# Performance work log

Hardware: AMD Instinct MI355X
Metric: run time of the kernel (lower is better)

## Reference

```python
import jax, jax.numpy as jnp
import numpy as np

B, P, D_IN, D_MOD, N_HEADS = 512, 64, 64, 256, 4

def _ln(x, g, b):
    m = x.mean(-1, keepdims=True)
    v = ((x - m) ** 2).mean(-1, keepdims=True)
    return (x - m) / jnp.sqrt(v + 1e-5) * g + b

def _lin(x, w, b):
    return x @ w.T + b

def _mha(q, k, v, in_w, in_b, out_w, out_b, n_heads):
    # Faithful to torch nn.MultiheadAttention(batch_first=False): dim0=seq, dim1=batch.
    S, N, E = q.shape
    dh = E // n_heads
    wq, wk, wv = jnp.split(in_w, 3, axis=0)
    bq, bk, bv = jnp.split(in_b, 3)
    qp = _lin(q, wq, bq).reshape(S, N, n_heads, dh)
    kp = _lin(k, wk, bk).reshape(S, N, n_heads, dh)
    vp = _lin(v, wv, bv).reshape(S, N, n_heads, dh)
    scores = jnp.einsum('snhd,tnhd->nhst', qp, kp) * (1.0 / np.sqrt(dh))
    attn = jax.nn.softmax(scores, axis=-1)
    o = jnp.einsum('nhst,tnhd->snhd', attn, vp).reshape(S, N, E)
    return _lin(o, out_w, out_b)

def _forward(x, emb_w, emb_b, emb_g, emb_beta, post_w, post_b, post_g, post_beta,
             attn_qw, attn_qb, attn_kw, attn_kb, attn_vw, attn_vb,
             attn_inw, attn_inb, attn_outw, attn_outb, attn_g, attn_beta,
             player_w, player_b, player_g, player_beta,
             team_w, team_b, team_g, team_beta,
             pre_w, pre_b, pre_g, pre_beta, lnf_g, lnf_b, pred_w, pred_b):
    # embedding: LinearWithLayerNorm = LayerNorm(Linear(x))
    p = _ln(_lin(x, emb_w, emb_b), emb_g, emb_beta)
    # post_embedding: ResidualLinearWithLayerNorm = LayerNorm(Linear(x)) + x
    p = _ln(_lin(p, post_w, post_b), post_g, post_beta) + p
    for i in range(2):
        res = p
        q = _lin(p, attn_qw[i], attn_qb[i])
        k = _lin(p, attn_kw[i], attn_kb[i])
        v = _lin(p, attn_vw[i], attn_vb[i])
        a = _mha(q, k, v, attn_inw[i], attn_inb[i], attn_outw[i], attn_outb[i], N_HEADS)
        p = _ln(a, attn_g[i], attn_beta[i]) + res
    for i in range(2):
        p = _ln(_lin(p, player_w[i], player_b[i]), player_g[i], player_beta[i]) + p
    # segment reduce: padded-ragged scatter + sum == masked sum over the player axis.
    # NOTE: original code computes BOTH masks as original[:,:,-1]==1 (bug preserved).
    mask = (x[:, :, -1] == 1).astype(p.dtype)  # [B, P]
    home = jnp.einsum('bpd,bp->bd', p, mask)
    away = home
    teams = jnp.concatenate([home, away], axis=1)  # [B, 2*d_mod]
    for i in range(2):
        teams = _ln(_lin(teams, team_w[i], team_b[i]), team_g[i], team_beta[i]) + teams
    o = _ln(_lin(teams, pre_w, pre_b), pre_g, pre_beta)
    o = _ln(o, lnf_g, lnf_b)
    o = _lin(o, pred_w, pred_b)[:, 0]  # squeeze(dim=1)
    return o


def setup_inputs() -> dict:
    key = jax.random.key(0)
    ks = iter(jax.random.split(key, 64))
    def nrm(shape):
        return jax.random.normal(next(ks), shape, jnp.float32) * 0.02
    x = jax.random.normal(next(ks), (B, P, D_IN), jnp.float32)
    flag = jax.random.bernoulli(next(ks), 0.5, (B, P)).astype(jnp.float32)
    x = x.at[:, :, -1].set(flag)  # binary home-team indicator channel
    d, d2 = D_MOD, 2 * D_MOD
    return dict(
        x=x,
        emb_w=nrm((d, D_IN)), emb_b=jnp.zeros(d), emb_g=jnp.ones(d), emb_beta=jnp.zeros(d),
        post_w=nrm((d, d)), post_b=jnp.zeros(d), post_g=jnp.ones(d), post_beta=jnp.zeros(d),
        attn_qw=nrm((2, d, d)), attn_qb=jnp.zeros((2, d)),
        attn_kw=nrm((2, d, d)), attn_kb=jnp.zeros((2, d)),
        attn_vw=nrm((2, d, d)), attn_vb=jnp.zeros((2, d)),
        attn_inw=nrm((2, 3 * d, d)), attn_inb=jnp.zeros((2, 3 * d)),
        attn_outw=nrm((2, d, d)), attn_outb=jnp.zeros((2, d)),
        attn_g=jnp.ones((2, d)), attn_beta=jnp.zeros((2, d)),
        player_w=nrm((2, d, d)), player_b=jnp.zeros((2, d)),
        player_g=jnp.ones((2, d)), player_beta=jnp.zeros((2, d)),
        team_w=nrm((2, d2, d2)), team_b=jnp.zeros((2, d2)),
        team_g=jnp.ones((2, d2)), team_beta=jnp.zeros((2, d2)),
        pre_w=nrm((d, d2)), pre_b=jnp.zeros(d), pre_g=jnp.ones(d), pre_beta=jnp.zeros(d),
        lnf_g=jnp.ones(d), lnf_b=jnp.zeros(d),
        pred_w=nrm((1, d)), pred_b=jnp.zeros(1),
    )


def reference(x, emb_w, emb_b, emb_g, emb_beta, post_w, post_b, post_g, post_beta,
              attn_qw, attn_qb, attn_kw, attn_kb, attn_vw, attn_vb,
              attn_inw, attn_inb, attn_outw, attn_outb, attn_g, attn_beta,
              player_w, player_b, player_g, player_beta,
              team_w, team_b, team_g, team_beta,
              pre_w, pre_b, pre_g, pre_beta, lnf_g, lnf_b, pred_w, pred_b):
    return _forward(x, emb_w, emb_b, emb_g, emb_beta, post_w, post_b, post_g, post_beta,
                    attn_qw, attn_qb, attn_kw, attn_kb, attn_vw, attn_vb,
                    attn_inw, attn_inb, attn_outw, attn_outb, attn_g, attn_beta,
                    player_w, player_b, player_g, player_beta,
                    team_w, team_b, team_g, team_beta,
                    pre_w, pre_b, pre_g, pre_beta, lnf_g, lnf_b, pred_w, pred_b)
```

## Files before the change

### kernel.cpp

```cpp
#include <hip/hip_runtime.h>
#include <math.h>


typedef __bf16 bf16x8 __attribute__((ext_vector_type(8)));
typedef __bf16 bf16x4 __attribute__((ext_vector_type(4)));
typedef __bf16 bf16x2 __attribute__((ext_vector_type(2)));
typedef float  f32x4  __attribute__((ext_vector_type(4)));
typedef unsigned short u16;
typedef unsigned short u16x8 __attribute__((ext_vector_type(8)));

__device__ __forceinline__ u16 f2b(float f) {
    unsigned int u = __builtin_bit_cast(unsigned int, f);
    return (u16)((u + 0x7fffu + ((u >> 16) & 1u)) >> 16);
}
__device__ __forceinline__ float b2f(u16 u) {
    unsigned int v = ((unsigned int)u) << 16;
    return __builtin_bit_cast(float, v);
}
__device__ __forceinline__ bf16x8 ld2x64(const u16* p) {
    bf16x4 lo = *(const bf16x4*)p;
    bf16x4 hi = *(const bf16x4*)(p + 4);
    return __builtin_shufflevector(lo, hi, 0, 1, 2, 3, 4, 5, 6, 7);
}
__device__ __forceinline__ bf16x8 ld4x32(const u16* p) {
    bf16x2 a = *(const bf16x2*)p,     b = *(const bf16x2*)(p + 2);
    bf16x2 c = *(const bf16x2*)(p + 4), d = *(const bf16x2*)(p + 6);
    bf16x4 lo = __builtin_shufflevector(a, b, 0, 1, 2, 3);
    bf16x4 hi = __builtin_shufflevector(c, d, 0, 1, 2, 3);
    return __builtin_shufflevector(lo, hi, 0, 1, 2, 3, 4, 5, 6, 7);
}
__device__ __forceinline__ void split8(const float* __restrict__ s,
                                       bf16x8& hi, bf16x8& lo) {
    u16x8 h, l;
    #pragma unroll
    for (int j = 0; j < 8; ++j) {
        float v  = s[j];
        u16  hb  = f2b(v);
        h[j] = hb;
        l[j] = f2b(v - b2f(hb));
    }
    hi = __builtin_bit_cast(bf16x8, h);
    lo = __builtin_bit_cast(bf16x8, l);
}

template<int IN, bool LN, bool RES, bool AF32, int OMODE, bool TEAM>
__device__ __forceinline__
void gemm_body(const void* __restrict__ Xa, const void* __restrict__ Xb, int ldX,
               const u16* __restrict__ Whi, const u16* __restrict__ Wlo,
               const float* __restrict__ bias,
               const float* __restrict__ g, const float* __restrict__ beta,
               const u16* __restrict__ resh, const u16* __restrict__ resl,
               int ldRes, void* __restrict__ Y0, void* __restrict__ Y1, int ldY,
               const float* __restrict__ xmask, float* __restrict__ teams,
               u16* __restrict__ Wb)
{
    constexpr int KT = IN / 32;
    const int tid = threadIdx.x;
    const int wv = tid >> 6, lane = tid & 63;
    const int quad = lane >> 4, l16 = lane & 15;
    const long arow = (long)blockIdx.x * 64 + wv * 16 + l16;

    const u16* sbase[8];
    int sdst[8];
    #pragma unroll
    for (int i = 0; i < 8; ++i) {
        int cid = tid + i * 256;
        int plane = cid >> 10, nt = (cid >> 6) & 15, slot = cid & 63;
        int q = slot >> 4, c = slot & 15;
        sbase[i] = (plane ? Wlo : Whi) + (long)(nt * 16 + c) * IN + q * 8;
        sdst[i]  = (plane * 16 + nt) * 512 + slot * 8;
    }
    u16x8 wreg[8];
    auto issueW = [&](int kt) {
        #pragma unroll
        for (int i = 0; i < 8; ++i) wreg[i] = *(const u16x8*)(sbase[i] + kt * 32);
    };
    auto commitW = [&](int buf) {
        #pragma unroll
        for (int i = 0; i < 8; ++i)
            *(u16x8*)&Wb[buf * 16384 + sdst[i]] = wreg[i];
    };

    bf16x8 ah[3], al[3];
    auto loadA = [&](int kt) {
        int s = kt % 3;
        long aofs = arow * (long)ldX + kt * 32 + quad * 8;
        if constexpr (AF32) {
            float av[8];
            *(f32x4*)&av[0] = *(const f32x4*)&((const float*)Xa)[aofs];
            *(f32x4*)&av[4] = *(const f32x4*)&((const float*)Xa)[aofs + 4];
            split8(av, ah[s], al[s]);
        } else {
            ah[s] = *(const bf16x8*)&((const u16*)Xa)[aofs];
            al[s] = *(const bf16x8*)&((const u16*)Xb)[aofs];
        }
    };

    f32x4 acc[16];
    #pragma unroll
    for (int nt = 0; nt < 16; ++nt) acc[nt] = f32x4{0.f, 0.f, 0.f, 0.f};

    issueW(0);
    commitW(0);
    if (KT > 1) issueW(1);
    loadA(0);
    if (KT > 1) loadA(1);
    __syncthreads();

    #pragma unroll
    for (int kt = 0; kt < KT; ++kt) {
        if (kt + 2 < KT) loadA(kt + 2);
        const u16* wb = Wb + (kt & 1) * 16384;
        const int s = kt % 3;
        #pragma unroll
        for (int nt = 0; nt < 16; ++nt) {
            bf16x8 bhi = *(const bf16x8*)&wb[nt * 512 + lane * 8];
            bf16x8 blo = *(const bf16x8*)&wb[(16 + nt) * 512 + lane * 8];
            acc[nt] = __builtin_amdgcn_mfma_f32_16x16x32_bf16(al[s], bhi, acc[nt], 0, 0, 0);
            acc[nt] = __builtin_amdgcn_mfma_f32_16x16x32_bf16(ah[s], blo, acc[nt], 0, 0, 0);
            acc[nt] = __builtin_amdgcn_mfma_f32_16x16x32_bf16(ah[s], bhi, acc[nt], 0, 0, 0);
        }
        if (kt + 1 < KT) {
            commitW((kt + 1) & 1);
            if (kt + 2 < KT) issueW(kt + 2);
            __syncthreads();
        }
    }

    #pragma unroll
    for (int nt = 0; nt < 16; ++nt) {
        float bc = bias[nt * 16 + l16];
        #pragma unroll
        for (int r = 0; r < 4; ++r) acc[nt][r] += bc;
    }

    float mean[4], rstd[4];
    if constexpr (LN) {
        float s1[4] = {0, 0, 0, 0}, s2[4] = {0, 0, 0, 0};
        #pragma unroll
        for (int nt = 0; nt < 16; ++nt)
            #pragma unroll
            for (int r = 0; r < 4; ++r) {
                s1[r] += acc[nt][r];
                s2[r] += acc[nt][r] * acc[nt][r];
            }
        #pragma unroll
        for (int off = 1; off < 16; off <<= 1)
            #pragma unroll
            for (int r = 0; r < 4; ++r) {
                s1[r] += __shfl_xor(s1[r], off, 64);
                s2[r] += __shfl_xor(s2[r], off, 64);
            }
        #pragma unroll
        for (int r = 0; r < 4; ++r) {
            mean[r] = s1[r] * (1.0f / 256.f);
            float var = s2[r] * (1.0f / 256.f) - mean[r] * mean[r];
            rstd[r] = rsqrtf(var + 1e-5f);
        }
    }

    if constexpr (TEAM) {
        float m[4];
        #pragma unroll
        for (int r = 0; r < 4; ++r) {
            long row = (long)blockIdx.x * 64 + wv * 16 + quad * 4 + r;
            m[r] = (xmask[row * 64 + 63] == 1.0f) ? 1.0f : 0.0f;
        }
        float ts[16];
        #pragma unroll
        for (int nt = 0; nt < 16; ++nt) {
            int col = nt * 16 + l16;
            float gc = g[col], bc2 = beta[col];
            ts[nt] = 0.f;
            #pragma unroll
            for (int r = 0; r < 4; ++r) {
                long row = (long)blockIdx.x * 64 + wv * 16 + quad * 4 + r;
                float v = (acc[nt][r] - mean[r]) * rstd[r] * gc + bc2;
                v += b2f(resh[row * ldRes + col]) + b2f(resl[row * ldRes + col]);
                ts[nt] += m[r] * v;
            }
        }
        #pragma unroll
        for (int nt = 0; nt < 16; ++nt) {
            ts[nt] += __shfl_xor(ts[nt], 16, 64);
            ts[nt] += __shfl_xor(ts[nt], 32, 64);
        }
        __syncthreads();
        float* tsum = (float*)Wb;
        if (quad == 0) {
            #pragma unroll
            for (int nt = 0; nt < 16; ++nt)
                tsum[wv * 256 + nt * 16 + l16] = ts[nt];
        }
        __syncthreads();
        if (tid < 256) {
            float tot = tsum[tid] + tsum[256 + tid]
                      + tsum[512 + tid] + tsum[768 + tid];
            teams[(long)blockIdx.x * 512 + tid]       = tot;
            teams[(long)blockIdx.x * 512 + 256 + tid] = tot;
        }
        return;
    }

    #pragma unroll
    for (int nt = 0; nt < 16; ++nt) {
        int col = nt * 16 + l16;
        float gc = 1.f, bc2 = 0.f;
        if constexpr (LN) { gc = g[col]; bc2 = beta[col]; }
        #pragma unroll
        for (int r = 0; r < 4; ++r) {
            long row = (long)blockIdx.x * 64 + wv * 16 + quad * 4 + r;
            float v = acc[nt][r];
            if constexpr (LN) v = (v - mean[r]) * rstd[r] * gc + bc2;
            if constexpr (RES)
                v += b2f(resh[row * ldRes + col]) + b2f(resl[row * ldRes + col]);
            long yofs = row * ldY + col;
            if constexpr (OMODE == 0) {
                ((float*)Y0)[yofs] = v;
            } else if constexpr (OMODE == 1) {
                u16 hb = f2b(v);
                ((u16*)Y0)[yofs] = hb;
                ((u16*)Y1)[yofs] = f2b(v - b2f(hb));
            } else if constexpr (OMODE == 2) {
                ((u16*)Y0)[yofs] = f2b(v);
            } else {
                long idx = ((long)((row & 63) * 4 + (col >> 6)) * 512
                            + (row >> 6)) * 64 + (col & 63);
                ((u16*)Y0)[idx] = f2b(v);
            }
        }
    }
}

template<int IN, bool LN, bool RES, bool AF32, int OMODE, bool TEAM>
__global__ __launch_bounds__(256)
void gemm_kernel(const void* __restrict__ Xa, const void* __restrict__ Xb, int ldX,
                 const u16* __restrict__ Whi, const u16* __restrict__ Wlo,
                 const float* __restrict__ bias,
                 const float* __restrict__ g, const float* __restrict__ beta,
                 const u16* __restrict__ resh, const u16* __restrict__ resl,
                 int ldRes, void* __restrict__ Y0, void* __restrict__ Y1, int ldY,
                 const float* __restrict__ xmask, float* __restrict__ teams)
{
    __shared__ u16 Wb[32768];
    gemm_body<IN, LN, RES, AF32, OMODE, TEAM>(Xa, Xb, ldX, Whi, Wlo, bias, g,
                                              beta, resh, resl, ldRes, Y0, Y1,
                                              ldY, xmask, teams, Wb);
}

__global__ __launch_bounds__(256)
void qkv_proj(const u16* __restrict__ ph, const u16* __restrict__ pl,
              const u16* __restrict__ cwL, const float* __restrict__ cb,
              u16* __restrict__ qb, u16* __restrict__ kb, u16* __restrict__ vh)
{
    __shared__ u16 Wb[32768];
    int wsel = blockIdx.y;
    const u16* whi = cwL + (long)wsel * 65536;
    const u16* wlo = cwL + 393216 + (long)wsel * 65536;
    u16* Y = (wsel == 0) ? qb : (wsel == 1) ? kb : vh;
    gemm_body<256, false, false, false, 3, false>(
        ph, pl, 256, whi, wlo, cb + wsel * 256, nullptr, nullptr,
        nullptr, nullptr, 0, Y, nullptr, 256, nullptr, nullptr, Wb);
}

__global__ __launch_bounds__(256)
void combine_kernel(const float* __restrict__ inw, const float* __restrict__ inb,
                    const float* __restrict__ qw, const float* __restrict__ kw,
                    const float* __restrict__ vw, const float* __restrict__ qb,
                    const float* __restrict__ kb, const float* __restrict__ vb,
                    u16* __restrict__ cw, float* __restrict__ cb)
{
    int idx = blockIdx.y, L = idx / 3, wsel = idx % 3;
    const float* Wa = inw + (long)L * 768 * 256 + wsel * 65536;
    const float* ba = inb + L * 768 + wsel * 256;
    const float* Wf = (wsel == 0 ? qw : wsel == 1 ? kw : vw) + (long)L * 65536;
    const float* bf = (wsel == 0 ? qb : wsel == 1 ? kb : vb) + L * 256;

    int o = blockIdx.x, j = threadIdx.x;
    float s = 0.f;
    for (int mm = 0; mm < 256; ++mm)
        s += Wa[o * 256 + mm] * Wf[mm * 256 + j];
    u16 hb = f2b(s);
    cw[(long)idx * 65536 + o * 256 + j] = hb;
    cw[393216 + (long)idx * 65536 + o * 256 + j] = f2b(s - b2f(hb));

    __shared__ float red[256];
    red[j] = Wa[o * 256 + j] * bf[j];
    __syncthreads();
    for (int st = 128; st > 0; st >>= 1) {
        if (j < st) red[j] += red[j + st];
        __syncthreads();
    }
    if (j == 0) cb[idx * 256 + o] = red[0] + ba[o];
}

__global__ __launch_bounds__(256)
void cast_split_multi(const float* s0, u16* d0, int n0,
                      const float* s1, u16* d1, int n1,
                      const float* s2, u16* d2, int n2,
                      const float* s3, u16* d3, int n3,
                      const float* s4, u16* d4, int n4,
                      const float* s5, u16* d5, int n5)
{
    const float* s; u16* d; int n;
    switch (blockIdx.y) {
        case 0: s = s0; d = d0; n = n0; break;
        case 1: s = s1; d = d1; n = n1; break;
        case 2: s = s2; d = d2; n = n2; break;
        case 3: s = s3; d = d3; n = n3; break;
        case 4: s = s4; d = d4; n = n4; break;
        default: s = s5; d = d5; n = n5; break;
    }
    int i = (blockIdx.x * 256 + threadIdx.x) * 4;
    if (i >= n) return;
    float4 v = *(const float4*)&s[i];
// ... 13 lines not shown
__global__ __launch_bounds__(256)
void attn_kernel(const u16* __restrict__ qbuf, const u16* __restrict__ kbuf,
                 const u16* __restrict__ vh,
                 u16* __restrict__ ofh, u16* __restrict__ ofl)
{
    const int n = blockIdx.x, h = blockIdx.y, sq = blockIdx.z;
    const int tid = threadIdx.x;
    const int wv = tid >> 6, lane = tid & 63;
    const int quad = lane >> 4, l16 = lane & 15;
    const long nhb = (long)(n * 4 + h) * 32768;

    __shared__ u16 Vth[64 * VTS];
    __shared__ u16 Pbh[4][32 * PS];

    bf16x8 qf[2][2];
    #pragma unroll
    for (int rt = 0; rt < 2; ++rt)
        #pragma unroll
        for (int kc = 0; kc < 2; ++kc) {
            long s = sq * 128 + wv * 32 + rt * 16 + l16;
            qf[rt][kc] = *(const bf16x8*)&qbuf[nhb + s * 64 + kc * 32 + quad * 8];
        }

    f32x4 o[2][4];
    #pragma unroll
    for (int rt = 0; rt < 2; ++rt)
        #pragma unroll
        for (int dt = 0; dt < 4; ++dt) o[rt][dt] = f32x4{0.f, 0.f, 0.f, 0.f};
    float l_run[2][4] = {{0.f, 0.f, 0.f, 0.f}, {0.f, 0.f, 0.f, 0.f}};

    for (int tb = 0; tb < 8; ++tb) {
        __syncthreads();
        for (int i = tid; i < 512; i += 256) {
            int t = i >> 3, c = i & 7;
            u16x8 hvv = *(const u16x8*)&vh[nhb + (long)(tb * 64 + t) * 64 + c * 8];
            #pragma unroll
            for (int j = 0; j < 8; ++j)
                Vth[(c * 8 + j) * VTS + t] = hvv[j];
        }
        __syncthreads();

        f32x4 sA[2][4];
        #pragma unroll
        for (int rt = 0; rt < 2; ++rt)
            #pragma unroll
            for (int tt = 0; tt < 4; ++tt) sA[rt][tt] = f32x4{0.f, 0.f, 0.f, 0.f};
        #pragma unroll
        for (int kc = 0; kc < 2; ++kc)
            #pragma unroll
            for (int tt = 0; tt < 4; ++tt) {
                bf16x8 kf = *(const bf16x8*)
                    &kbuf[nhb + (long)(tb * 64 + tt * 16 + l16) * 64
                          + kc * 32 + quad * 8];
                sA[0][tt] = __builtin_amdgcn_mfma_f32_16x16x32_bf16(
                    qf[0][kc], kf, sA[0][tt], 0, 0, 0);
                sA[1][tt] = __builtin_amdgcn_mfma_f32_16x16x32_bf16(
                    qf[1][kc], kf, sA[1][tt], 0, 0, 0);
            }

        #pragma unroll
        for (int rt = 0; rt < 2; ++rt)
            #pragma unroll
            for (int r = 0; r < 4; ++r) {
                float p0 = exp2f(sA[rt][0][r] * EXP2SCALE);
                float p1 = exp2f(sA[rt][1][r] * EXP2SCALE);
                float p2 = exp2f(sA[rt][2][r] * EXP2SCALE);
                float p3 = exp2f(sA[rt][3][r] * EXP2SCALE);
                int prow = (rt * 16 + quad * 4 + r) * PS + l16;
                Pbh[wv][prow +  0] = f2b(p0);
                Pbh[wv][prow + 16] = f2b(p1);
                Pbh[wv][prow + 32] = f2b(p2);
                Pbh[wv][prow + 48] = f2b(p3);
                l_run[rt][r] += (p0 + p1) + (p2 + p3);
            }

        #pragma unroll
        for (int kc = 0; kc < 2; ++kc) {
            bf16x8 pfh[2];
            #pragma unroll
            for (int rt = 0; rt < 2; ++rt)
                pfh[rt] = ld2x64(&Pbh[wv][(rt * 16 + l16) * PS
                                          + kc * 32 + quad * 8]);
            #pragma unroll
            for (int dt = 0; dt < 4; ++dt) {
                bf16x8 vfh = ld4x32(&Vth[(dt * 16 + l16) * VTS
                                         + kc * 32 + quad * 8]);
                o[0][dt] = __builtin_amdgcn_mfma_f32_16x16x32_bf16(
                    pfh[0], vfh, o[0][dt], 0, 0, 0);
                o[1][dt] = __builtin_amdgcn_mfma_f32_16x16x32_bf16(
                    pfh[1], vfh, o[1][dt], 0, 0, 0);
            }
        }
    }

    #pragma unroll
    for (int off = 1; off < 16; off <<= 1)
        #pragma unroll
        for (int rt = 0; rt < 2; ++rt)
            #pragma unroll
            for (int r = 0; r < 4; ++r)
                l_run[rt][r] += __shfl_xor(l_run[rt][r], off, 64);

    #pragma unroll
    for (int rt = 0; rt < 2; ++rt)
        #pragma unroll
        for (int r = 0; r < 4; ++r) {
            float inv = 1.0f / l_run[rt][r];
            long s = sq * 128 + wv * 32 + rt * 16 + quad * 4 + r;
            #pragma unroll
            for (int dt = 0; dt < 4; ++dt) {
                long idx = (s * 64 + n) * 256 + h * 64 + dt * 16 + l16;
                float val = o[rt][dt][r] * inv;
                u16 hb = f2b(val);
                ofh[idx] = hb;
                ofl[idx] = f2b(val - b2f(hb));
            }
        }
}

template<int IN, int OUT, bool RES>
__global__ __launch_bounds__(256)
void tail_gemm(const float* __restrict__ X,
               const u16* __restrict__ Whi, const u16* __restrict__ Wlo,
               const float* __restrict__ bias,
               const float* __restrict__ g, const float* __restrict__ beta,
               const float* __restrict__ res, float* __restrict__ Y)
{
    constexpr int NTW = OUT / 64;
    constexpr int KT  = IN / 32;
    const int tid = threadIdx.x;
    const int wv = tid >> 6, lane = tid & 63;
    const int quad = lane >> 4, l16 = lane & 15;
    const int row0 = blockIdx.x * 16;
    const int colbase = wv * (OUT / 4);

    f32x4 acc[NTW];
    #pragma unroll
    for (int nt = 0; nt < NTW; ++nt) acc[nt] = f32x4{0.f, 0.f, 0.f, 0.f};

    #pragma unroll
    for (int kt = 0; kt < KT; ++kt) {
        float av[8];
        long aofs = (long)(row0 + l16) * IN + kt * 32 + quad * 8;
        *(f32x4*)&av[0] = *(const f32x4*)&X[aofs];
        *(f32x4*)&av[4] = *(const f32x4*)&X[aofs + 4];
        bf16x8 ah, al;
        split8(av, ah, al);
        #pragma unroll
        for (int nt = 0; nt < NTW; ++nt) {
            long wofs = (long)(colbase + nt * 16 + l16) * IN + kt * 32 + quad * 8;
            bf16x8 bhi = *(const bf16x8*)&Whi[wofs];
            bf16x8 blo = *(const bf16x8*)&Wlo[wofs];
            acc[nt] = __builtin_amdgcn_mfma_f32_16x16x32_bf16(al, bhi, acc[nt], 0, 0, 0);
            acc[nt] = __builtin_amdgcn_mfma_f32_16x16x32_bf16(ah, blo, acc[nt], 0, 0, 0);
            acc[nt] = __builtin_amdgcn_mfma_f32_16x16x32_bf16(ah, bhi, acc[nt], 0, 0, 0);
        }
    }

    #pragma unroll
    for (int nt = 0; nt < NTW; ++nt) {
        float bc = bias[colbase + nt * 16 + l16];
        #pragma unroll
        for (int r = 0; r < 4; ++r) acc[nt][r] += bc;
    }

    float s1[4] = {0, 0, 0, 0}, s2[4] = {0, 0, 0, 0};
    #pragma unroll
    for (int nt = 0; nt < NTW; ++nt)
        #pragma unroll
        for (int r = 0; r < 4; ++r) {
            s1[r] += acc[nt][r];
            s2[r] += acc[nt][r] * acc[nt][r];
        }
    #pragma unroll
    for (int off = 1; off < 16; off <<= 1)
        #pragma unroll
        for (int r = 0; r < 4; ++r) {
            s1[r] += __shfl_xor(s1[r], off, 64);
            s2[r] += __shfl_xor(s2[r], off, 64);
        }
    __shared__ float r1[64], r2[64];
    if (l16 == 0) {
        #pragma unroll
        for (int r = 0; r < 4; ++r) {
            r1[wv * 16 + quad * 4 + r] = s1[r];
            r2[wv * 16 + quad * 4 + r] = s2[r];
        }
    }
    __syncthreads();
    float mean[4], rstd[4];
    #pragma unroll
    for (int r = 0; r < 4; ++r) {
        int rr = quad * 4 + r;
        float t1 = r1[rr] + r1[16 + rr] + r1[32 + rr] + r1[48 + rr];
        float t2 = r2[rr] + r2[16 + rr] + r2[32 + rr] + r2[48 + rr];
        mean[r] = t1 * (1.0f / OUT);
        float var = t2 * (1.0f / OUT) - mean[r] * mean[r];
        rstd[r] = rsqrtf(var + 1e-5f);
    }
    #pragma unroll
    for (int nt = 0; nt < NTW; ++nt) {
        int col = colbase + nt * 16 + l16;
        float gc = g[col], bc2 = beta[col];
        #pragma unroll
        for (int r = 0; r < 4; ++r) {
            int row = row0 + quad * 4 + r;
            float v = (acc[nt][r] - mean[r]) * rstd[r] * gc + bc2;
            if constexpr (RES) v += res[(long)row * OUT + col];
            Y[(long)row * OUT + col] = v;
        }
    }
}

__global__ __launch_bounds__(256)
void tail_pred(const float* __restrict__ X,
               const u16* __restrict__ Whi, const u16* __restrict__ Wlo,
               const float* __restrict__ bias,
               const float* __restrict__ g, const float* __restrict__ beta,
               const float* __restrict__ lnf_g, const float* __restrict__ lnf_b,
               const float* __restrict__ pw, const float* __restrict__ pb,
               float* __restrict__ out)
{
    constexpr int IN = 512, OUT = 256, NTW = 4, KT = 16;
    const int tid = threadIdx.x;
    const int wv = tid >> 6, lane = tid & 63;
    const int quad = lane >> 4, l16 = lane & 15;
    const int row0 = blockIdx.x * 16;
    const int colbase = wv * 64;

    f32x4 acc[NTW];
    #pragma unroll
    for (int nt = 0; nt < NTW; ++nt) acc[nt] = f32x4{0.f, 0.f, 0.f, 0.f};

    #pragma unroll
    for (int kt = 0; kt < KT; ++kt) {
        float av[8];
        long aofs = (long)(row0 + l16) * IN + kt * 32 + quad * 8;
        *(f32x4*)&av[0] = *(const f32x4*)&X[aofs];
        *(f32x4*)&av[4] = *(const f32x4*)&X[aofs + 4];
        bf16x8 ah, al;
        split8(av, ah, al);
        #pragma unroll
        for (int nt = 0; nt < NTW; ++nt) {
            long wofs = (long)(colbase + nt * 16 + l16) * IN + kt * 32 + quad * 8;
            bf16x8 bhi = *(const bf16x8*)&Whi[wofs];
            bf16x8 blo = *(const bf16x8*)&Wlo[wofs];
            acc[nt] = __builtin_amdgcn_mfma_f32_16x16x32_bf16(al, bhi, acc[nt], 0, 0, 0);
            acc[nt] = __builtin_amdgcn_mfma_f32_16x16x32_bf16(ah, blo, acc[nt], 0, 0, 0);
            acc[nt] = __builtin_amdgcn_mfma_f32_16x16x32_bf16(ah, bhi, acc[nt], 0, 0, 0);
        }
    }
    #pragma unroll
    for (int nt = 0; nt < NTW; ++nt) {
        float bc = bias[colbase + nt * 16 + l16];
        #pragma unroll
        for (int r = 0; r < 4; ++r) acc[nt][r] += bc;
    }

    __shared__ float r1[64], r2[64];
    float s1[4] = {0, 0, 0, 0}, s2[4] = {0, 0, 0, 0};
    #pragma unroll
    for (int nt = 0; nt < NTW; ++nt)
        #pragma unroll
        for (int r = 0; r < 4; ++r) {
            s1[r] += acc[nt][r];
            s2[r] += acc[nt][r] * acc[nt][r];
        }
    #pragma unroll
    for (int off = 1; off < 16; off <<= 1)
        #pragma unroll
        for (int r = 0; r < 4; ++r) {
            s1[r] += __shfl_xor(s1[r], off, 64);
            s2[r] += __shfl_xor(s2[r], off, 64);
        }
    if (l16 == 0)
        #pragma unroll
        for (int r = 0; r < 4; ++r) {
            r1[wv * 16 + quad * 4 + r] = s1[r];
            r2[wv * 16 + quad * 4 + r] = s2[r];
        }
    __syncthreads();
    float vv[NTW][4];
    #pragma unroll
    for (int r = 0; r < 4; ++r) {
        int rr = quad * 4 + r;
        float t1 = r1[rr] + r1[16 + rr] + r1[32 + rr] + r1[48 + rr];
        float t2 = r2[rr] + r2[16 + rr] + r2[32 + rr] + r2[48 + rr];
        float mean = t1 * (1.0f / OUT);
        float rstd = rsqrtf(t2 * (1.0f / OUT) - mean * mean + 1e-5f);
        #pragma unroll
        for (int nt = 0; nt < NTW; ++nt) {
            int col = colbase + nt * 16 + l16;
            vv[nt][r] = (acc[nt][r] - mean) * rstd * g[col] + beta[col];
        }
    }
    float u1[4] = {0, 0, 0, 0}, u2[4] = {0, 0, 0, 0};
    #pragma unroll
    for (int nt = 0; nt < NTW; ++nt)
        #pragma unroll
        for (int r = 0; r < 4; ++r) {
            u1[r] += vv[nt][r];
            u2[r] += vv[nt][r] * vv[nt][r];
// ... 74 lines not shown
    const float* attn_outw = (const float*)d_in[17];
    const float* attn_outb = (const float*)d_in[18];
    const float* attn_g    = (const float*)d_in[19];
    const float* attn_beta = (const float*)d_in[20];
    const float* player_w  = (const float*)d_in[21];
    const float* player_b  = (const float*)d_in[22];
    const float* player_g  = (const float*)d_in[23];
    const float* player_bt = (const float*)d_in[24];
    const float* team_w    = (const float*)d_in[25];
    const float* team_b    = (const float*)d_in[26];
    const float* team_g    = (const float*)d_in[27];
    const float* team_beta = (const float*)d_in[28];
    const float* pre_w     = (const float*)d_in[29];
    const float* pre_b     = (const float*)d_in[30];
    const float* pre_g     = (const float*)d_in[31];
    const float* pre_beta  = (const float*)d_in[32];
    const float* lnf_g     = (const float*)d_in[33];
    const float* lnf_b     = (const float*)d_in[34];
    const float* pred_w    = (const float*)d_in[35];
    const float* pred_b    = (const float*)d_in[36];

    char* base = (char*)d_ws;
    const size_t NR = (size_t)32768 * 256;
    u16* ph  = (u16*)base;  base += NR * 2;
    u16* pl  = (u16*)base;  base += NR * 2;
    u16* ofh = (u16*)base;  base += NR * 2;
    u16* ofl = (u16*)base;  base += NR * 2;
    u16* vh  = (u16*)base;  base += NR * 2;
    u16* qb  = (u16*)base;  base += NR * 2;
    u16* kb  = (u16*)base;  base += NR * 2;
    float* teams0 = (float*)base; base += (size_t)512 * 512 * 4;
    float* teams1 = (float*)base; base += (size_t)512 * 512 * 4;
    u16* emb_wp    = (u16*)base;  base += (size_t)2 * 16384 * 2;
    u16* post_wp   = (u16*)base;  base += (size_t)2 * 65536 * 2;
    u16* outw_p    = (u16*)base;  base += (size_t)2 * 131072 * 2;
    u16* player_wp = (u16*)base;  base += (size_t)2 * 131072 * 2;
    u16* team_wp   = (u16*)base;  base += (size_t)2 * 524288 * 2;
    u16* pre_wp    = (u16*)base;  base += (size_t)2 * 131072 * 2;
    u16* cwb       = (u16*)base;  base += (size_t)2 * 393216 * 2;
    float* cbf     = (float*)base; base += (size_t)1536 * 4;

    cast_split_multi<<<dim3(512, 6), 256, 0, stream>>>(
        emb_w, emb_wp, 16384,
        post_w, post_wp, 65536,
        attn_outw, outw_p, 131072,
        player_w, player_wp, 131072,
        team_w, team_wp, 524288,
        pre_w, pre_wp, 131072);

    combine_kernel<<<dim3(256, 6), 256, 0, stream>>>(
        attn_inw, attn_inb, attn_qw, attn_kw, attn_vw,
        attn_qb, attn_kb, attn_vb, cwb, cbf);

    gemm_kernel<64, true, false, true, 1, false><<<512, 256, 0, stream>>>(
        x, nullptr, 64, emb_wp, emb_wp + 16384, emb_b, emb_g, emb_beta,
        nullptr, nullptr, 0, ph, pl, 256, nullptr, nullptr);
    gemm_kernel<256, true, true, false, 1, false><<<512, 256, 0, stream>>>(
        ph, pl, 256, post_wp, post_wp + 65536, post_b, post_g, post_beta,
        ph, pl, 256, ph, pl, 256, nullptr, nullptr);

    for (int L = 0; L < 2; ++L) {
        qkv_proj<<<dim3(512, 3), 256, 0, stream>>>(
            ph, pl, cwb + (size_t)L * 3 * 65536, cbf + L * 768, qb, kb, vh);
        attn_kernel<<<dim3(64, 4, 4), 256, 0, stream>>>(qb, kb, vh, ofh, ofl);
        gemm_kernel<256, true, true, false, 1, false><<<512, 256, 0, stream>>>(
            ofh, ofl, 256, outw_p + (size_t)L * 65536,
            outw_p + 131072 + (size_t)L * 65536, attn_outb + L * 256,
            attn_g + L * 256, attn_beta + L * 256, ph, pl, 256, ph, pl, 256,
            nullptr, nullptr);
    }

    gemm_kernel<256, true, true, false, 1, false><<<512, 256, 0, stream>>>(
        ph, pl, 256, player_wp, player_wp + 131072, player_b,
        player_g, player_bt, ph, pl, 256, ph, pl, 256, nullptr, nullptr);
    gemm_kernel<256, true, true, false, 1, true><<<512, 256, 0, stream>>>(
        ph, pl, 256, player_wp + 65536, player_wp + 131072 + 65536,
        player_b + 256, player_g + 256, player_bt + 256, ph, pl, 256,
        nullptr, nullptr, 256, x, teams0);

    tail_gemm<512, 512, true><<<32, 256, 0, stream>>>(
        teams0, team_wp, team_wp + 524288, team_b,
        team_g, team_beta, teams0, teams1);
    tail_gemm<512, 512, true><<<32, 256, 0, stream>>>(
        teams1, team_wp + 262144, team_wp + 524288 + 262144, team_b + 512,
        team_g + 512, team_beta + 512, teams1, teams0);

    tail_pred<<<32, 256, 0, stream>>>(
        teams0, pre_wp, pre_wp + 131072, pre_b, pre_g, pre_beta,
        lnf_g, lnf_b, pred_w, pred_b, (float*)d_out);
}
```

Before: 745.4 us.

## Fuse per-row GEMM chains into three kernels with in-register activation reuse

Merges the embedding, post-embedding, QKV projections, out-projection and player layers into three fused kernels. Each block keeps its 64-row tile and moves outputs between stages through a shared-memory transpose into A-fragments, so intermediates are not reloaded from global memory. This cuts kernel launches and A-operand traffic. The trade-off is that the QKV projections run serially within one block rather than as a 3x grid, which reduces parallelism, and register pressure rises from holding 16 A-fragments.

After: 790.4 us. 1.06x slower.

```diff
diff --git a/kernel.cpp b/kernel.cpp
--- a/kernel.cpp
+++ b/kernel.cpp
@@ -43,123 +43,360 @@
     lo = __builtin_bit_cast(bf16x8, l);
 }
 
-template<int IN, bool LN, bool RES, bool AF32, int OMODE, bool TEAM>
-__device__ __forceinline__
-void gemm_body(const void* __restrict__ Xa, const void* __restrict__ Xb, int ldX,
-               const u16* __restrict__ Whi, const u16* __restrict__ Wlo,
-               const float* __restrict__ bias,
-               const float* __restrict__ g, const float* __restrict__ beta,
-               const u16* __restrict__ resh, const u16* __restrict__ resl,
-               int ldRes, void* __restrict__ Y0, void* __restrict__ Y1, int ldY,
-               const float* __restrict__ xmask, float* __restrict__ teams,
-               u16* __restrict__ Wb)
-{
-    constexpr int KT = IN / 32;
+#define MFMA __builtin_amdgcn_mfma_f32_16x16x32_bf16
+
+
+struct WCtx { const u16* sbase[8]; int sdst[8]; };
+
+__device__ __forceinline__ void wctx_init(WCtx& c, const u16* Whi,
+                                          const u16* Wlo, int tid) {
+    #pragma unroll
+    for (int i = 0; i < 8; ++i) {
+        int cid = tid + i * 256;
+        int plane = cid >> 10, nt = (cid >> 6) & 15, slot = cid & 63;
+        int q = slot >> 4, cc = slot & 15;
+        c.sbase[i] = (plane ? Wlo : Whi) + (long)(nt * 16 + cc) * 256 + q * 8;
+        c.sdst[i]  = (plane * 16 + nt) * 512 + slot * 8;
+    }
+}
+
+__device__ __forceinline__ void stage256_reg(
+    const bf16x8 Ah[8], const bf16x8 Al[8],
+    const u16* __restrict__ Whi, const u16* __restrict__ Wlo,
+    u16* __restrict__ Wb, int tid, int lane, f32x4 acc[16])
+{
+    WCtx c; wctx_init(c, Whi, Wlo, tid);
+    u16x8 wreg[8];
+    auto issueW = [&](int kt) {
+        #pragma unroll
+        for (int i = 0; i < 8; ++i) wreg[i] = *(const u16x8*)(c.sbase[i] + kt * 32);
+    };
+    auto commitW = [&](int buf) {
+        #pragma unroll
+        for (int i = 0; i < 8; ++i)
+            *(u16x8*)&Wb[buf * 16384 + c.sdst[i]] = wreg[i];
+    };
+    #pragma unroll
+    for (int nt = 0; nt < 16; ++nt) acc[nt] = f32x4{0.f, 0.f, 0.f, 0.f};
+    __syncthreads();
+    issueW(0); commitW(0); issueW(1);
+    __syncthreads();
+    #pragma unroll
+    for (int kt = 0; kt < 8; ++kt) {
+        const u16* wb = Wb + (kt & 1) * 16384;
+        #pragma unroll
+        for (int nt = 0; nt < 16; ++nt) {
+            bf16x8 bhi = *(const bf16x8*)&wb[nt * 512 + lane * 8];
+            bf16x8 blo = *(const bf16x8*)&wb[(16 + nt) * 512 + lane * 8];
+            acc[nt] = MFMA(Al[kt], bhi, acc[nt], 0, 0, 0);
+            acc[nt] = MFMA(Ah[kt], blo, acc[nt], 0, 0, 0);
+            acc[nt] = MFMA(Ah[kt], bhi, acc[nt], 0, 0, 0);
+        }
+        if (kt + 1 < 8) {
+            commitW((kt + 1) & 1);
+            if (kt + 2 < 8) issueW(kt + 2);
+            __syncthreads();
+        }
+    }
+}
+
+__device__ __forceinline__ void stage256_gA(
+    const u16* __restrict__ Xa, const u16* __restrict__ Xb,
+    const u16* __restrict__ Whi, const u16* __restrict__ Wlo,
+    u16* __restrict__ Wb, int tid, int wv, int lane, int quad, int l16,
+    f32x4 acc[16])
+{
+    WCtx c; wctx_init(c, Whi, Wlo, tid);
+    const long arow = (long)blockIdx.x * 64 + wv * 16 + l16;
+    u16x8 wreg[8];
+    auto issueW = [&](int kt) {
+        #pragma unroll
+        for (int i = 0; i < 8; ++i) wreg[i] = *(const u16x8*)(c.sbase[i] + kt * 32);
+    };
+    auto commitW = [&](int buf) {
+        #pragma unroll
+        for (int i = 0; i < 8; ++i)
+            *(u16x8*)&Wb[buf * 16384 + c.sdst[i]] = wreg[i];
+    };
+    bf16x8 ah[3], al[3];
+    auto loadA = [&](int kt) {
+        int s = kt % 3;
+        long aofs = arow * 256 + kt * 32 + quad * 8;
+        ah[s] = *(const bf16x8*)&Xa[aofs];
+        al[s] = *(const bf16x8*)&Xb[aofs];
+    };
+    #pragma unroll
+    for (int nt = 0; nt < 16; ++nt) acc[nt] = f32x4{0.f, 0.f, 0.f, 0.f};
+    issueW(0); commitW(0); issueW(1);
+    loadA(0); loadA(1);
+    __syncthreads();
+    #pragma unroll
+    for (int kt = 0; kt < 8; ++kt) {
+        if (kt + 2 < 8) loadA(kt + 2);
+        const u16* wb = Wb + (kt & 1) * 16384;
+        const int s = kt % 3;
+        #pragma unroll
+        for (int nt = 0; nt < 16; ++nt) {
+            bf16x8 bhi = *(const bf16x8*)&wb[nt * 512 + lane * 8];
+            bf16x8 blo = *(const bf16x8*)&wb[(16 + nt) * 512 + lane * 8];
+            acc[nt] = MFMA(al[s], bhi, acc[nt], 0, 0, 0);
+            acc[nt] = MFMA(ah[s], blo, acc[nt], 0, 0, 0);
+            acc[nt] = MFMA(ah[s], bhi, acc[nt], 0, 0, 0);
+        }
+        if (kt + 1 < 8) {
+            commitW((kt + 1) & 1);
+            if (kt + 2 < 8) issueW(kt + 2);
+            __syncthreads();
+        }
+    }
+}
+
+__device__ __forceinline__ void xpose(const f32x4 acc[16], u16* __restrict__ Wb,
+                                      int wv, int quad, int l16,
+                                      bf16x8 Ah[8], bf16x8 Al[8])
+{
+    u16* Xw = Wb + wv * (16 * 264);
+    __syncthreads();
+    #pragma unroll
+    for (int nt = 0; nt < 16; ++nt)
+        #pragma unroll
+        for (int r = 0; r < 4; ++r)
+            Xw[(quad * 4 + r) * 264 + nt * 16 + l16] = f2b(acc[nt][r]);
+    #pragma unroll
+    for (int kt = 0; kt < 8; ++kt)
+        Ah[kt] = *(const bf16x8*)&Xw[l16 * 264 + kt * 32 + quad * 8];
+    #pragma unroll
+    for (int nt = 0; nt < 16; ++nt)
+        #pragma unroll
+        for (int r = 0; r < 4; ++r) {
+            float v = acc[nt][r];
+            u16 hb = f2b(v);
+            Xw[(quad * 4 + r) * 264 + nt * 16 + l16] = f2b(v - b2f(hb));
+        }
+    #pragma unroll
+    for (int kt = 0; kt < 8; ++kt)
+        Al[kt] = *(const bf16x8*)&Xw[l16 * 264 + kt * 32 + quad * 8];
+}
+
+__device__ __forceinline__ void ln_stats(const f32x4 acc[16],
+                                         float mean[4], float rstd[4])
+{
+    float s1[4] = {0, 0, 0, 0}, s2[4] = {0, 0, 0, 0};
+    #pragma unroll
+    for (int nt = 0; nt < 16; ++nt)
+        #pragma unroll
+        for (int r = 0; r < 4; ++r) {
+            s1[r] += acc[nt][r];
+            s2[r] += acc[nt][r] * acc[nt][r];
+        }
+    #pragma unroll
+    for (int off = 1; off < 16; off <<= 1)
+        #pragma unroll
+        for (int r = 0; r < 4; ++r) {
+            s1[r] += __shfl_xor(s1[r], off, 64);
+            s2[r] += __shfl_xor(s2[r], off, 64);
+        }
+    #pragma unroll
+    for (int r = 0; r < 4; ++r) {
+        mean[r] = s1[r] * (1.0f / 256.f);
+        float var = s2[r] * (1.0f / 256.f) - mean[r] * mean[r];
+        rstd[r] = rsqrtf(var + 1e-5f);
+    }
+}
+
+template<bool RES>
+__device__ __forceinline__ void epi_ln_store(f32x4 acc[16],
+    const float* __restrict__ bias, const float* __restrict__ g,
+    const float* __restrict__ beta, u16* __restrict__ ph, u16* __restrict__ pl,
+    int wv, int quad, int l16)
+{
+    #pragma unroll
+    for (int nt = 0; nt < 16; ++nt) {
+        float bc = bias[nt * 16 + l16];
+        #pragma unroll
+        for (int r = 0; r < 4; ++r) acc[nt][r] += bc;
+    }
+    float mean[4], rstd[4];
+    ln_stats(acc, mean, rstd);
+    #pragma unroll
+    for (int nt = 0; nt < 16; ++nt) {
+        int col = nt * 16 + l16;
+        float gc = g[col], bc2 = beta[col];
+        #pragma unroll
+        for (int r = 0; r < 4; ++r) {
+            long row = (long)blockIdx.x * 64 + wv * 16 + quad * 4 + r;
+            float v = (acc[nt][r] - mean[r]) * rstd[r] * gc + bc2;
+            if constexpr (RES)
+                v += b2f(ph[row * 256 + col]) + b2f(pl[row * 256 + col]);
+            acc[nt][r] = v;
+            u16 hb = f2b(v);
+            ph[row * 256 + col] = hb;
+            pl[row * 256 + col] = f2b(v - b2f(hb));
+        }
+    }
+}
+
+__device__ __forceinline__ void epi_qkv(const f32x4 acc[16],
+    const float* __restrict__ bias, u16* __restrict__ Y,
+    int wv, int quad, int l16)
+{
+    #pragma unroll
+    for (int nt = 0; nt < 16; ++nt) {
+        int col = nt * 16 + l16;
+        float bc = bias[col];
+        #pragma unroll
+        for (int r = 0; r < 4; ++r) {
+            long row = (long)blockIdx.x * 64 + wv * 16 + quad * 4 + r;
+            float v = acc[nt][r] + bc;
+            long idx = ((long)((row & 63) * 4 + (col >> 6)) * 512
+                        + (row >> 6)) * 64 + (col & 63);
+            Y[idx] = f2b(v);
+        }
+    }
+}
+
+__global__ __launch_bounds__(256)
+void fused_k1(const float* __restrict__ x,
+              const u16* __restrict__ emb_wp, const float* __restrict__ emb_b,
+              const float* __restrict__ emb_g, const float* __restrict__ emb_bt,
+              const u16* __restrict__ post_wp, const float* __restrict__ post_b,
+              const float* __restrict__ post_g, const float* __restrict__ post_bt,
+              const u16* __restrict__ cwb, const float* __restrict__ cbf,
+              u16* __restrict__ ph, u16* __restrict__ pl,
+              u16* __restrict__ qb, u16* __restrict__ kb, u16* __restrict__ vh)
+{
+    __shared__ u16 Wb[32768];
     const int tid = threadIdx.x;
     const int wv = tid >> 6, lane = tid & 63;
     const int quad = lane >> 4, l16 = lane & 15;
-    const long arow = (long)blockIdx.x * 64 + wv * 16 + l16;
-
-    const u16* sbase[8];
-    int sdst[8];
-    #pragma unroll
-    for (int i = 0; i < 8; ++i) {
-        int cid = tid + i * 256;
-        int plane = cid >> 10, nt = (cid >> 6) & 15, slot = cid & 63;
-        int q = slot >> 4, c = slot & 15;
-        sbase[i] = (plane ? Wlo : Whi) + (long)(nt * 16 + c) * IN + q * 8;
-        sdst[i]  = (plane * 16 + nt) * 512 + slot * 8;
-    }
-    u16x8 wreg[8];
-    auto issueW = [&](int kt) {
-        #pragma unroll
-        for (int i = 0; i < 8; ++i) wreg[i] = *(const u16x8*)(sbase[i] + kt * 32);
-    };
-    auto commitW = [&](int buf) {
-        #pragma unroll
-        for (int i = 0; i < 8; ++i)
-            *(u16x8*)&Wb[buf * 16384 + sdst[i]] = wreg[i];
-    };
-
-    bf16x8 ah[3], al[3];
-    auto loadA = [&](int kt) {
-        int s = kt % 3;
-        long aofs = arow * (long)ldX + kt * 32 + quad * 8;
-        if constexpr (AF32) {
+
+    f32x4 acc[16];
+    {
+        #pragma unroll
+        for (int i = 0; i < 16; ++i) {
+            int cid = tid + i * 256;
+            int kt = cid >> 11;
+            int c2 = cid & 2047;
+            int plane = c2 >> 10, nt = (c2 >> 6) & 15, slot = c2 & 63;
+            int q = slot >> 4, cc = slot & 15;
+            const u16* src = emb_wp + plane * 16384
+                           + (long)(nt * 16 + cc) * 64 + kt * 32 + q * 8;
+            *(u16x8*)&Wb[kt * 16384 + (plane * 16 + nt) * 512 + slot * 8] =
+                *(const u16x8*)src;
+        }
+        bf16x8 eh[2], el[2];
+        #pragma unroll
+        for (int kt = 0; kt < 2; ++kt) {
             float av[8];
-            *(f32x4*)&av[0] = *(const f32x4*)&((const float*)Xa)[aofs];
-            *(f32x4*)&av[4] = *(const f32x4*)&((const float*)Xa)[aofs + 4];
-            split8(av, ah[s], al[s]);
-        } else {
-            ah[s] = *(const bf16x8*)&((const u16*)Xa)[aofs];
-            al[s] = *(const bf16x8*)&((const u16*)Xb)[aofs];
-        }
-    };
+            long aofs = ((long)blockIdx.x * 64 + wv * 16 + l16) * 64
+                      + kt * 32 + quad * 8;
+            *(f32x4*)&av[0] = *(const f32x4*)&x[aofs];
+            *(f32x4*)&av[4] = *(const f32x4*)&x[aofs + 4];
+            split8(av, eh[kt], el[kt]);
+        }
+        #pragma unroll
+        for (int nt = 0; nt < 16; ++nt) acc[nt] = f32x4{0.f, 0.f, 0.f, 0.f};
+        __syncthreads();
+        #pragma unroll
+        for (int kt = 0; kt < 2; ++kt) {
+            const u16* wb = Wb + kt * 16384;
+            #pragma unroll
+            for (int nt = 0; nt < 16; ++nt) {
+                bf16x8 bhi = *(const bf16x8*)&wb[nt * 512 + lane * 8];
+                bf16x8 blo = *(const bf16x8*)&wb[(16 + nt) * 512 + lane * 8];
+                acc[nt] = MFMA(el[kt], bhi, acc[nt], 0, 0, 0);
+                acc[nt] = MFMA(eh[kt], blo, acc[nt], 0, 0, 0);
+                acc[nt] = MFMA(eh[kt], bhi, acc[nt], 0, 0, 0);
+            }
+        }
+    }
+    epi_ln_store<false>(acc, emb_b, emb_g, emb_bt, ph, pl, wv, quad, l16);
+
+    bf16x8 Ah[8], Al[8];
+    xpose(acc, Wb, wv, quad, l16, Ah, Al);
+    stage256_reg(Ah, Al, post_wp, post_wp + 65536, Wb, tid, lane, acc);
+    epi_ln_store<true>(acc, post_b, post_g, post_bt, ph, pl, wv, quad, l16);
+
+    xpose(acc, Wb, wv, quad, l16, Ah, Al);
+    u16* Ys[3] = {qb, kb, vh};
+    #pragma unroll 1
+    for (int wsel = 0; wsel < 3; ++wsel) {
+        const u16* whi = cwb + (long)wsel * 65536;
+        const u16* wlo = cwb + 393216 + (long)wsel * 65536;
+        stage256_reg(Ah, Al, whi, wlo, Wb, tid, lane, acc);
+        epi_qkv(acc, cbf + wsel * 256, Ys[wsel], wv, quad, l16);
+    }
+}
+
+__global__ __launch_bounds__(256)
+void fused_k2(const u16* __restrict__ ofh, const u16* __restrict__ ofl,
+              const u16* __restrict__ outw_hi, const u16* __restrict__ outw_lo,
+              const float* __restrict__ outb, const float* __restrict__ og,
+              const float* __restrict__ obt,
+              const u16* __restrict__ cwL, const float* __restrict__ cbL,
+              u16* __restrict__ ph, u16* __restrict__ pl,
+              u16* __restrict__ qb, u16* __restrict__ kb, u16* __restrict__ vh)
+{
+    __shared__ u16 Wb[32768];
+    const int tid = threadIdx.x;
+    const int wv = tid >> 6, lane = tid & 63;
+    const int quad = lane >> 4, l16 = lane & 15;
 
     f32x4 acc[16];
-    #pragma unroll
-    for (int nt = 0; nt < 16; ++nt) acc[nt] = f32x4{0.f, 0.f, 0.f, 0.f};
-
-    issueW(0);
-    commitW(0);
-    if (KT > 1) issueW(1);
-    loadA(0);
-    if (KT > 1) loadA(1);
-    __syncthreads();
-
-    #pragma unroll
-    for (int kt = 0; kt < KT; ++kt) {
-        if (kt + 2 < KT) loadA(kt + 2);
-        const u16* wb = Wb + (kt & 1) * 16384;
-        const int s = kt % 3;
+    stage256_gA(ofh, ofl, outw_hi, outw_lo, Wb, tid, wv, lane, quad, l16, acc);
+    epi_ln_store<true>(acc, outb, og, obt, ph, pl, wv, quad, l16);
+
+    bf16x8 Ah[8], Al[8];
+    xpose(acc, Wb, wv, quad, l16, Ah, Al);
+    u16* Ys[3] = {qb, kb, vh};
+    #pragma unroll 1
+    for (int wsel = 0; wsel < 3; ++wsel) {
+        const u16* whi = cwL + (long)wsel * 65536;
+        const u16* wlo = cwL + 393216 + (long)wsel * 65536;
+        stage256_reg(Ah, Al, whi, wlo, Wb, tid, lane, acc);
+        epi_qkv(acc, cbL + wsel * 256, Ys[wsel], wv, quad, l16);
+    }
+}
+
+__global__ __launch_bounds__(256)
+void fused_k3(const u16* __restrict__ ofh, const u16* __restrict__ ofl,
+              const u16* __restrict__ outw_hi, const u16* __restrict__ outw_lo,
+              const float* __restrict__ outb, const float* __restrict__ og,
+              const float* __restrict__ obt,
+              const u16* __restrict__ player_wp, const float* __restrict__ player_b,
+              const float* __restrict__ player_g, const float* __restrict__ player_bt,
+              const float* __restrict__ xmask, float* __restrict__ teams,
+              u16* __restrict__ ph, u16* __restrict__ pl)
+{
+    __shared__ u16 Wb[32768];
+    const int tid = threadIdx.x;
+    const int wv = tid >> 6, lane = tid & 63;
+    const int quad = lane >> 4, l16 = lane & 15;
+
+    f32x4 acc[16];
+    stage256_gA(ofh, ofl, outw_hi, outw_lo, Wb, tid, wv, lane, quad, l16, acc);
+    epi_ln_store<true>(acc, outb, og, obt, ph, pl, wv, quad, l16);
+
+    bf16x8 Ah[8], Al[8];
+    xpose(acc, Wb, wv, quad, l16, Ah, Al);
+    stage256_reg(Ah, Al, player_wp, player_wp + 131072, Wb, tid, lane, acc);
+    epi_ln_store<true>(acc, player_b, player_g, player_bt, ph, pl, wv, quad, l16);
+
+    xpose(acc, Wb, wv, quad, l16, Ah, Al);
+    stage256_reg(Ah, Al, player_wp + 65536, player_wp + 131072 + 65536,
+                 Wb, tid, lane, acc);
+    {
+        const float* bias = player_b + 256;
+        const float* g    = player_g + 256;
+        const float* beta = player_bt + 256;
         #pragma unroll
         for (int nt = 0; nt < 16; ++nt) {
-            bf16x8 bhi = *(const bf16x8*)&wb[nt * 512 + lane * 8];
-            bf16x8 blo = *(const bf16x8*)&wb[(16 + nt) * 512 + lane * 8];
-            acc[nt] = __builtin_amdgcn_mfma_f32_16x16x32_bf16(al[s], bhi, acc[nt], 0, 0, 0);
-            acc[nt] = __builtin_amdgcn_mfma_f32_16x16x32_bf16(ah[s], blo, acc[nt], 0, 0, 0);
-            acc[nt] = __builtin_amdgcn_mfma_f32_16x16x32_bf16(ah[s], bhi, acc[nt], 0, 0, 0);
-        }
-        if (kt + 1 < KT) {
-            commitW((kt + 1) & 1);
-            if (kt + 2 < KT) issueW(kt + 2);
-            __syncthreads();
-        }
-    }
-
-    #pragma unroll
-    for (int nt = 0; nt < 16; ++nt) {
-        float bc = bias[nt * 16 + l16];
-        #pragma unroll
-        for (int r = 0; r < 4; ++r) acc[nt][r] += bc;
-    }
-
-    float mean[4], rstd[4];
-    if constexpr (LN) {
-        float s1[4] = {0, 0, 0, 0}, s2[4] = {0, 0, 0, 0};
-        #pragma unroll
-        for (int nt = 0; nt < 16; ++nt)
-            #pragma unroll
-            for (int r = 0; r < 4; ++r) {
-                s1[r] += acc[nt][r];
-                s2[r] += acc[nt][r] * acc[nt][r];
-            }
-        #pragma unroll
-        for (int off = 1; off < 16; off <<= 1)
-            #pragma unroll
-            for (int r = 0; r < 4; ++r) {
-                s1[r] += __shfl_xor(s1[r], off, 64);
-                s2[r] += __shfl_xor(s2[r], off, 64);
-            }
-        #pragma unroll
-        for (int r = 0; r < 4; ++r) {
-            mean[r] = s1[r] * (1.0f / 256.f);
-            float var = s2[r] * (1.0f / 256.f) - mean[r] * mean[r];
-            rstd[r] = rsqrtf(var + 1e-5f);
-        }
-    }
-
-    if constexpr (TEAM) {
+            float bc = bias[nt * 16 + l16];
+            #pragma unroll
+            for (int r = 0; r < 4; ++r) acc[nt][r] += bc;
+        }
+        float mean[4], rstd[4];
+        ln_stats(acc, mean, rstd);
         float m[4];
         #pragma unroll
         for (int r = 0; r < 4; ++r) {
@@ -176,7 +413,7 @@
             for (int r = 0; r < 4; ++r) {
                 long row = (long)blockIdx.x * 64 + wv * 16 + quad * 4 + r;
                 float v = (acc[nt][r] - mean[r]) * rstd[r] * gc + bc2;
-                v += b2f(resh[row * ldRes + col]) + b2f(resl[row * ldRes + col]);
+                v += b2f(ph[row * 256 + col]) + b2f(pl[row * 256 + col]);
                 ts[nt] += m[r] * v;
             }
         }
@@ -199,68 +436,7 @@
             teams[(long)blockIdx.x * 512 + tid]       = tot;
             teams[(long)blockIdx.x * 512 + 256 + tid] = tot;
         }
-        return;
-    }
-
-    #pragma unroll
-    for (int nt = 0; nt < 16; ++nt) {
-        int col = nt * 16 + l16;
-        float gc = 1.f, bc2 = 0.f;
-        if constexpr (LN) { gc = g[col]; bc2 = beta[col]; }
-        #pragma unroll
-        for (int r = 0; r < 4; ++r) {
-            long row = (long)blockIdx.x * 64 + wv * 16 + quad * 4 + r;
-            float v = acc[nt][r];
-            if constexpr (LN) v = (v - mean[r]) * rstd[r] * gc + bc2;
-            if constexpr (RES)
-                v += b2f(resh[row * ldRes + col]) + b2f(resl[row * ldRes + col]);
-            long yofs = row * ldY + col;
-            if constexpr (OMODE == 0) {
-                ((float*)Y0)[yofs] = v;
-            } else if constexpr (OMODE == 1) {
-                u16 hb = f2b(v);
-                ((u16*)Y0)[yofs] = hb;
-                ((u16*)Y1)[yofs] = f2b(v - b2f(hb));
-            } else if constexpr (OMODE == 2) {
-                ((u16*)Y0)[yofs] = f2b(v);
-            } else {
-                long idx = ((long)((row & 63) * 4 + (col >> 6)) * 512
-                            + (row >> 6)) * 64 + (col & 63);
-                ((u16*)Y0)[idx] = f2b(v);
-            }
-        }
-    }
-}
-
-template<int IN, bool LN, bool RES, bool AF32, int OMODE, bool TEAM>
-__global__ __launch_bounds__(256)
-void gemm_kernel(const void* __restrict__ Xa, const void* __restrict__ Xb, int ldX,
-                 const u16* __restrict__ Whi, const u16* __restrict__ Wlo,
-                 const float* __restrict__ bias,
-                 const float* __restrict__ g, const float* __restrict__ beta,
-                 const u16* __restrict__ resh, const u16* __restrict__ resl,
-                 int ldRes, void* __restrict__ Y0, void* __restrict__ Y1, int ldY,
-                 const float* __restrict__ xmask, float* __restrict__ teams)
-{
-    __shared__ u16 Wb[32768];
-    gemm_body<IN, LN, RES, AF32, OMODE, TEAM>(Xa, Xb, ldX, Whi, Wlo, bias, g,
-                                              beta, resh, resl, ldRes, Y0, Y1,
-                                              ldY, xmask, teams, Wb);
-}
-
-__global__ __launch_bounds__(256)
-void qkv_proj(const u16* __restrict__ ph, const u16* __restrict__ pl,
-              const u16* __restrict__ cwL, const float* __restrict__ cb,
-              u16* __restrict__ qb, u16* __restrict__ kb, u16* __restrict__ vh)
-{
-    __shared__ u16 Wb[32768];
-    int wsel = blockIdx.y;
-    const u16* whi = cwL + (long)wsel * 65536;
-    const u16* wlo = cwL + 393216 + (long)wsel * 65536;
-    u16* Y = (wsel == 0) ? qb : (wsel == 1) ? kb : vh;
-    gemm_body<256, false, false, false, 3, false>(
-        ph, pl, 256, whi, wlo, cb + wsel * 256, nullptr, nullptr,
-        nullptr, nullptr, 0, Y, nullptr, 256, nullptr, nullptr, Wb);
+    }
 }
 
 __global__ __launch_bounds__(256)
@@ -380,10 +556,8 @@
                 bf16x8 kf = *(const bf16x8*)
                     &kbuf[nhb + (long)(tb * 64 + tt * 16 + l16) * 64
                           + kc * 32 + quad * 8];
-                sA[0][tt] = __builtin_amdgcn_mfma_f32_16x16x32_bf16(
-                    qf[0][kc], kf, sA[0][tt], 0, 0, 0);
-                sA[1][tt] = __builtin_amdgcn_mfma_f32_16x16x32_bf16(
-                    qf[1][kc], kf, sA[1][tt], 0, 0, 0);
+                sA[0][tt] = MFMA(qf[0][kc], kf, sA[0][tt], 0, 0, 0);
+                sA[1][tt] = MFMA(qf[1][kc], kf, sA[1][tt], 0, 0, 0);
             }
 
         #pragma unroll
@@ -413,10 +587,8 @@
             for (int dt = 0; dt < 4; ++dt) {
                 bf16x8 vfh = ld4x32(&Vth[(dt * 16 + l16) * VTS
                                          + kc * 32 + quad * 8]);
-                o[0][dt] = __builtin_amdgcn_mfma_f32_16x16x32_bf16(
-                    pfh[0], vfh, o[0][dt], 0, 0, 0);
-                o[1][dt] = __builtin_amdgcn_mfma_f32_16x16x32_bf16(
-                    pfh[1], vfh, o[1][dt], 0, 0, 0);
+                o[0][dt] = MFMA(pfh[0], vfh, o[0][dt], 0, 0, 0);
+                o[1][dt] = MFMA(pfh[1], vfh, o[1][dt], 0, 0, 0);
             }
         }
     }
@@ -479,9 +651,9 @@
             long wofs = (long)(colbase + nt * 16 + l16) * IN + kt * 32 + quad * 8;
             bf16x8 bhi = *(const bf16x8*)&Whi[wofs];
             bf16x8 blo = *(const bf16x8*)&Wlo[wofs];
-            acc[nt] = __builtin_amdgcn_mfma_f32_16x16x32_bf16(al, bhi, acc[nt], 0, 0, 0);
-            acc[nt] = __builtin_amdgcn_mfma_f32_16x16x32_bf16(ah, blo, acc[nt], 0, 0, 0);
-            acc[nt] = __builtin_amdgcn_mfma_f32_16x16x32_bf16(ah, bhi, acc[nt], 0, 0, 0);
+            acc[nt] = MFMA(al, bhi, acc[nt], 0, 0, 0);
+            acc[nt] = MFMA(ah, blo, acc[nt], 0, 0, 0);
+            acc[nt] = MFMA(ah, bhi, acc[nt], 0, 0, 0);
         }
     }
 
@@ -573,9 +745,9 @@
             long wofs = (long)(colbase + nt * 16 + l16) * IN + kt * 32 + quad * 8;
             bf16x8 bhi = *(const bf16x8*)&Whi[wofs];
             bf16x8 blo = *(const bf16x8*)&Wlo[wofs];
-            acc[nt] = __builtin_amdgcn_mfma_f32_16x16x32_bf16(al, bhi, acc[nt], 0, 0, 0);
-            acc[nt] = __builtin_amdgcn_mfma_f32_16x16x32_bf16(ah, blo, acc[nt], 0, 0, 0);
-            acc[nt] = __builtin_amdgcn_mfma_f32_16x16x32_bf16(ah, bhi, acc[nt], 0, 0, 0);
+            acc[nt] = MFMA(al, bhi, acc[nt], 0, 0, 0);
+            acc[nt] = MFMA(ah, blo, acc[nt], 0, 0, 0);
+            acc[nt] = MFMA(ah, bhi, acc[nt], 0, 0, 0);
         }
     }
     #pragma unroll
@@ -756,31 +928,24 @@
         attn_inw, attn_inb, attn_qw, attn_kw, attn_vw,
         attn_qb, attn_kb, attn_vb, cwb, cbf);
 
-    gemm_kernel<64, true, false, true, 1, false><<<512, 256, 0, stream>>>(
-        x, nullptr, 64, emb_wp, emb_wp + 16384, emb_b, emb_g, emb_beta,
-        nullptr, nullptr, 0, ph, pl, 256, nullptr, nullptr);
-    gemm_kernel<256, true, true, false, 1, false><<<512, 256, 0, stream>>>(
-        ph, pl, 256, post_wp, post_wp + 65536, post_b, post_g, post_beta,
-        ph, pl, 256, ph, pl, 256, nullptr, nullptr);
-
-    for (int L = 0; L < 2; ++L) {
-        qkv_proj<<<dim3(512, 3), 256, 0, stream>>>(
-            ph, pl, cwb + (size_t)L * 3 * 65536, cbf + L * 768, qb, kb, vh);
-        attn_kernel<<<dim3(64, 4, 4), 256, 0, stream>>>(qb, kb, vh, ofh, ofl);
-        gemm_kernel<256, true, true, false, 1, false><<<512, 256, 0, stream>>>(
-            ofh, ofl, 256, outw_p + (size_t)L * 65536,
-            outw_p + 131072 + (size_t)L * 65536, attn_outb + L * 256,
-            attn_g + L * 256, attn_beta + L * 256, ph, pl, 256, ph, pl, 256,
-            nullptr, nullptr);
-    }
-
-    gemm_kernel<256, true, true, false, 1, false><<<512, 256, 0, stream>>>(
-        ph, pl, 256, player_wp, player_wp + 131072, player_b,
-        player_g, player_bt, ph, pl, 256, ph, pl, 256, nullptr, nullptr);
-    gemm_kernel<256, true, true, false, 1, true><<<512, 256, 0, stream>>>(
-        ph, pl, 256, player_wp + 65536, player_wp + 131072 + 65536,
-        player_b + 256, player_g + 256, player_bt + 256, ph, pl, 256,
-        nullptr, nullptr, 256, x, teams0);
+    fused_k1<<<512, 256, 0, stream>>>(
+        x, emb_wp, emb_b, emb_g, emb_beta,
+        post_wp, post_b, post_g, post_beta,
+        cwb, cbf, ph, pl, qb, kb, vh);
+
+    attn_kernel<<<dim3(64, 4, 4), 256, 0, stream>>>(qb, kb, vh, ofh, ofl);
+
+    fused_k2<<<512, 256, 0, stream>>>(
+        ofh, ofl, outw_p, outw_p + 131072, attn_outb, attn_g, attn_beta,
+        cwb + (size_t)3 * 65536, cbf + 768, ph, pl, qb, kb, vh);
+
+    attn_kernel<<<dim3(64, 4, 4), 256, 0, stream>>>(qb, kb, vh, ofh, ofl);
+
+    fused_k3<<<512, 256, 0, stream>>>(
+        ofh, ofl, outw_p + 65536, outw_p + 131072 + 65536,
+        attn_outb + 256, attn_g + 256, attn_beta + 256,
+        player_wp, player_b, player_g, player_bt,
+        x, teams0, ph, pl);
 
     tail_gemm<512, 512, true><<<32, 256, 0, stream>>>(
         teams0, team_wp, team_wp + 524288, team_b,
```
